# Kernel tuning notes

Hardware: AMD Instinct MI355X
Metric: run time of the kernel (lower is better)

## Reference

```python
import jax, jax.numpy as jnp
import numpy as np

TOPK = 2  # config.expert_topk


def setup_inputs() -> dict:
    key = jax.random.key(0)
    k1, k2, k3, k4 = jax.random.split(key, 4)
    B, T, D, H, E = 2, 2048, 768, 3072, 8
    x = jax.random.normal(k1, (B, T, D), jnp.float32)
    gate_w = jax.random.normal(k2, (E, D), jnp.float32) * 0.02   # nn.Linear(D, E).weight
    w_fc = jax.random.normal(k3, (E, H, D), jnp.float32) * 0.02  # per-expert c_fc.weight [out,in]
    w_proj = jax.random.normal(k4, (E, D, H), jnp.float32) * 0.02  # per-expert c_proj.weight
    return {"x": x, "gate_w": gate_w, "w_fc": w_fc, "w_proj": w_proj}


def reference(x, gate_w, w_fc, w_proj):
    # x: [B,T,D]; gate_w: [E,D]; w_fc: [E,H,D]; w_proj: [E,D,H]
    B, T, D = x.shape
    E = gate_w.shape[0]
    N = B * T
    xf = x.reshape(N, D)

    gate_logits = xf @ gate_w.T                       # [N,E]
    gate_probs = jax.nn.softmax(gate_logits, axis=-1)
    rw, idx = jax.lax.top_k(gate_probs, TOPK)          # [N,k]
    rw = rw / jnp.sum(rw, axis=-1, keepdims=True)

    # combine[n,e] = sum_k rw[n,k] * (idx[n,k]==e); zero for unselected experts,
    # so the dense per-expert MLP below computes the same math as torch dispatch.
    oh = jax.nn.one_hot(idx, E, dtype=xf.dtype)        # [N,k,E]
    combine = jnp.einsum('nk,nke->ne', rw, oh)         # [N,E]

    h = jnp.einsum('nd,ehd->neh', xf, w_fc)            # [N,E,H]
    h = jnp.square(jax.nn.relu(h))                     # relu(x)^2
    y = jnp.einsum('neh,edh->ned', h, w_proj)          # [N,E,D]
    out = jnp.einsum('ned,ne->nd', y, combine).reshape(B, T, D)

    # expert_freq = bincount(expert_indices)/N, detached in the loss
    counts = jnp.sum(oh, axis=(0, 1))                  # [E]
    expert_freq = counts / N
    balance_loss = jnp.sum(gate_probs.mean(axis=0) * jax.lax.stop_gradient(expert_freq)) * E
    return out, balance_loss
```

## Files before the change

kernel.cpp:

```cpp
#include <hip/hip_runtime.h>
#include <hip/hip_bf16.h>

typedef __bf16 bf16_t;
typedef bf16_t bf16x8 __attribute__((ext_vector_type(8)));
typedef bf16_t bf16x4 __attribute__((ext_vector_type(4)));
typedef float f32x4 __attribute__((ext_vector_type(4)));

#define N_TOK 4096
#define DIM   768
#define HID   3072
#define NEXP  8
#define PADROWS 9216
#define MMAX  32
#define MT2   64

#define OFF_COUNTS 0
#define OFF_PSUM   32
#define OFF_OFFPAD 64
#define OFF_CURSOR 128
#define OFF_TOKE   256
#define OFF_TOKW   (OFF_TOKE + 4*8192)
#define OFF_PERMT  (OFF_TOKW + 4*8192)
#define OFF_PERMW  (OFF_PERMT + 4*PADROWS)
#define OFF_XP     (((OFF_PERMW + 4*PADROWS) + 511) & ~511ull)
#define OFF_WFC    (OFF_XP + 2ull*PADROWS*DIM)
#define OFF_WPJ    (OFF_WFC + 2ull*NEXP*HID*DIM)
#define OFF_H      (OFF_WPJ + 2ull*NEXP*DIM*HID)
#define WS_NEEDED  (OFF_H + 2ull*PADROWS*HID)

#define GATE_BLOCKS (N_TOK / 4)
#define CONVH_BLOCKS 4608
#define GEMM1_BLOCKS (8 * 24 * MMAX)

__device__ __forceinline__ void async_copy16(const bf16_t* g, bf16_t* l) {
    __builtin_amdgcn_global_load_lds(
        (const __attribute__((address_space(1))) void*)g,
        (__attribute__((address_space(3))) void*)l, 16, 0, 0);
}

__device__ __forceinline__ void convert_chunk(const float* __restrict__ src,
                                              bf16_t* __restrict__ dst,
                                              int cid, int t) {
    const long long base = (long long)cid * 256 + t;
    const long long stride = (long long)CONVH_BLOCKS * 256;
#pragma unroll
    for (int it = 0; it < 4; it++) {
        const long long i4 = base + (long long)it * stride;
        float4 v = *((const float4*)src + i4);
        bf16x4 o;
        o[0] = (bf16_t)v.x; o[1] = (bf16_t)v.y;
        o[2] = (bf16_t)v.z; o[3] = (bf16_t)v.w;
        *(bf16x4*)(dst + i4 * 4) = o;
    }
}

__global__ __launch_bounds__(256) void prep_kernel(
    const float* __restrict__ w_fc, bf16_t* __restrict__ wfc_b,
    const float* __restrict__ x, const float* __restrict__ gw,
    int* __restrict__ cs_part, float* __restrict__ ps_part,
    int* __restrict__ tok_e, float* __restrict__ tok_w)
{
    __shared__ float ps[8];
    __shared__ int cs[8];

    if (blockIdx.x >= GATE_BLOCKS) {
        convert_chunk(w_fc, wfc_b, blockIdx.x - GATE_BLOCKS, threadIdx.x);
        return;
    }

    if (threadIdx.x < 8) { ps[threadIdx.x] = 0.f; cs[threadIdx.x] = 0; }
    __syncthreads();

    const int bid = blockIdx.x;
    const int wv = threadIdx.x >> 6, lane = threadIdx.x & 63;
    const int n = bid * 4 + wv;

    float acc[8];
#pragma unroll
    for (int e = 0; e < 8; e++) acc[e] = 0.f;
    const float* xr = x + (size_t)n * DIM;
#pragma unroll
    for (int c = 0; c < 12; c++) {
        const float xv = xr[c * 64 + lane];
#pragma unroll
        for (int e = 0; e < 8; e++) acc[e] += xv * gw[e * DIM + c * 64 + lane];
    }
#pragma unroll
    for (int e = 0; e < 8; e++)
        for (int off = 32; off > 0; off >>= 1) acc[e] += __shfl_xor(acc[e], off, 64);

    float mx = acc[0];
#pragma unroll
    for (int e = 1; e < 8; e++) mx = fmaxf(mx, acc[e]);
    float p[8], s = 0.f;
#pragma unroll
    for (int e = 0; e < 8; e++) { p[e] = expf(acc[e] - mx); s += p[e]; }

    int e1 = 0;
#pragma unroll
    for (int e = 1; e < 8; e++) if (p[e] > p[e1]) e1 = e;
    int e2 = (e1 == 0) ? 1 : 0;
#pragma unroll
    for (int e = 0; e < 8; e++) if (e != e1 && p[e] > p[e2]) e2 = e;
    const float denom = p[e1] + p[e2];

    if (lane == 0) {
        tok_e[2 * n] = e1; tok_e[2 * n + 1] = e2;
        tok_w[2 * n] = p[e1] / denom; tok_w[2 * n + 1] = p[e2] / denom;
        const float inv = 1.f / s;
#pragma unroll
        for (int e = 0; e < 8; e++) atomicAdd(&ps[e], p[e] * inv);
        atomicAdd(&cs[e1], 1); atomicAdd(&cs[e2], 1);
    }
    __syncthreads();
    if (threadIdx.x < 8) {
        ps_part[bid * 8 + threadIdx.x] = ps[threadIdx.x];
        cs_part[bid * 8 + threadIdx.x] = cs[threadIdx.x];
    }
}

__global__ __launch_bounds__(256) void finalize_scatter(
    const int* cs_part, const float* ps_part,
    const int* __restrict__ tok_e, const float* __restrict__ tok_w,
    int* __restrict__ counts, int* __restrict__ off_pad,
    int* perm_tok, int* inv_pos, float* __restrict__ out_loss)
{
    __shared__ float rps[256];
    __shared__ int rcs[256];
    __shared__ int s_cur[8];
    const int t = threadIdx.x;
    const int e = t & 7, chunk = t >> 3;
    float psum = 0.f; int csum = 0;
#pragma unroll
    for (int i = 0; i < 32; i++) {
        const int b = chunk * 32 + i;
        psum += ps_part[b * 8 + e];
        csum += cs_part[b * 8 + e];
    }
    rps[t] = psum; rcs[t] = csum;
    __syncthreads();
    for (int s = 128; s >= 8; s >>= 1) {
        if (t < s) { rps[t] += rps[t + s]; rcs[t] += rcs[t + s]; }
        __syncthreads();
    }
    if (t == 0) {
        int off = 0; float loss = 0.f;
        for (int k = 0; k < 8; k++) {
            counts[k] = rcs[k];
            off_pad[k] = off; s_cur[k] = off;
            off += ((rcs[k] + 127) & ~127);
            loss += rps[k] * (float)rcs[k];
        }
        off_pad[8] = off;
        *out_loss = loss * 8.f / ((float)N_TOK * (float)N_TOK);
    }
    __syncthreads();
    for (int r = 0; r < N_TOK / 256; r++) {
        const int n = r * 256 + t;
#pragma unroll
        for (int k = 0; k < 2; k++) {
            const int ee = tok_e[2 * n + k];
            const int pos = atomicAdd(&s_cur[ee], 1);
            perm_tok[pos] = n;
            inv_pos[2 * n + k] = pos;
        }
    }
}

__global__ __launch_bounds__(256) void gather_x_kernel(
    const float* __restrict__ x, const int* __restrict__ off_pad,
    const int* __restrict__ counts, const int* __restrict__ perm_tok,
    bf16_t* __restrict__ xp)
{
    __shared__ int so[9], scnt[8];
    if (threadIdx.x < 9) so[threadIdx.x] = off_pad[threadIdx.x];
    if (threadIdx.x < 8) scnt[threadIdx.x] = counts[threadIdx.x];
    __syncthreads();
    const int gid = blockIdx.x * 256 + threadIdx.x;
    const int p = gid / 192;
    const int c = (gid - p * 192) * 4;
    int e = 0;
#pragma unroll
    for (int k = 1; k < 8; k++) if (p >= so[k]) e = k;
    const bool valid = (p < so[8]) && (p - so[e] < scnt[e]);
    float4 v = make_float4(0.f, 0.f, 0.f, 0.f);
    if (valid) {
        const int tok = perm_tok[p];
        v = *(const float4*)(x + (size_t)tok * DIM + c);
    }
    bf16x4 o; o[0] = (bf16_t)v.x; o[1] = (bf16_t)v.y; o[2] = (bf16_t)v.z; o[3] = (bf16_t)v.w;
    *(bf16x4*)(xp + (size_t)p * DIM + c) = o;
}

__global__ __launch_bounds__(256, 3) void gemm1_kernel(
    const bf16_t* __restrict__ xp, const bf16_t* __restrict__ wfc,
    const int* __restrict__ off_pad, bf16_t* __restrict__ h,
    const float* __restrict__ w_proj, bf16_t* __restrict__ wpj_b)
{
    const int id = blockIdx.x;
    if (id >= GEMM1_BLOCKS) {
        convert_chunk(w_proj, wpj_b, id - GEMM1_BLOCKS, threadIdx.x);
        return;
    }
    const int e = id & 7;
    const int slot = id >> 3;
    const int n_t = slot / MMAX, m_t = slot % MMAX;

    const int seg0 = off_pad[e];
    const int cnt_pad = off_pad[e + 1] - seg0;
    const int m0 = m_t * 128;
    if (m0 >= cnt_pad) return;
    const int n0 = n_t * 128;

    __shared__ bf16_t As[128 * 64];
    __shared__ bf16_t Bs[128 * 64];

    const int t = threadIdx.x;
    const int srow = t >> 3, sc = t & 7;
    const int gsc = sc ^ (srow & 7);
    const bf16_t* abase = xp + (size_t)(seg0 + m0 + srow) * DIM + gsc * 8;
    const bf16_t* bbase = wfc + ((size_t)e * HID + n0 + srow) * DIM + gsc * 8;

    const int wv = t >> 6, lane = t & 63;
    const int lrow = lane & 15, quad = lane >> 4;
    const int wm = (wv & 1) * 64, wn = (wv >> 1) * 64;
    const int sw = lrow & 7;

    f32x4 acc[4][4] = {};

    for (int k0 = 0; k0 < DIM; k0 += 64) {
        __syncthreads();
#pragma unroll
        for (int ii = 0; ii < 4; ii++) {
            async_copy16(abase + (size_t)ii * 32 * DIM + k0, &As[(ii * 256 + t) * 8]);
            async_copy16(bbase + (size_t)ii * 32 * DIM + k0, &Bs[(ii * 256 + t) * 8]);
        }
        __syncthreads();
#pragma unroll
        for (int kh = 0; kh < 2; kh++) {
            const int ch = ((kh * 4 + quad) ^ sw) * 8;
            bf16x8 af[4], bfv[4];
#pragma unroll
            for (int i = 0; i < 4; i++)
                af[i] = *(bf16x8*)&As[(wm + i * 16 + lrow) * 64 + ch];
#pragma unroll
            for (int j = 0; j < 4; j++)
                bfv[j] = *(bf16x8*)&Bs[(wn + j * 16 + lrow) * 64 + ch];
#pragma unroll
            for (int i = 0; i < 4; i++)
#pragma unroll
                for (int j = 0; j < 4; j++)
                    acc[i][j] = __builtin_amdgcn_mfma_f32_16x16x32_bf16(af[i], bfv[j], acc[i][j], 0, 0, 0);
        }
    }

#pragma unroll
    for (int i = 0; i < 4; i++) {
#pragma unroll
        for (int g = 0; g < 4; g++) {
            const int m = m0 + wm + i * 16 + quad * 4 + g;
            bf16_t* hrow = h + (size_t)(seg0 + m) * HID + n0 + wn + lrow;
#pragma unroll
            for (int j = 0; j < 4; j++) {
                float v = fmaxf(acc[i][j][g], 0.f);
                hrow[j * 16] = (bf16_t)(v * v);
            }
        }
    }
}

__global__ __launch_bounds__(256, 3) void gemm2_kernel(
    const bf16_t* __restrict__ h, const bf16_t* __restrict__ wpj,
    const int* __restrict__ off_pad, const int* __restrict__ counts,
    bf16_t* __restrict__ y)
{
    const int id = blockIdx.x;
    const int e = id & 7;
    const int slot = id >> 3;
    const int m_t = slot / 6, n_t = slot % 6;

    const int seg0 = off_pad[e];
    const int cnt = counts[e];
    const int m0 = m_t * 64;
    if (m0 >= cnt) return;
    const int n0 = n_t * 128;

    __shared__ bf16_t As[2][64 * 64];
    __shared__ bf16_t Bs[2][128 * 64];

    const int t = threadIdx.x;
    const int srow = t >> 3, sc = t & 7;
    const int gsc = sc ^ (srow & 7);
    const bf16_t* abase = h + (size_t)(seg0 + m0 + srow) * HID + gsc * 8;
    const bf16_t* bbase = wpj + ((size_t)e * DIM + n0 + srow) * HID + gsc * 8;

    const int wv = t >> 6, lane = t & 63;
    const int lrow = lane & 15, quad = lane >> 4;
    const int wm = (wv & 1) * 32, wn = (wv >> 1) * 64;
    const int sw = lrow & 7;

    f32x4 acc[2][4] = {};

    for (int k0 = 0; k0 < HID; k0 += 128) {
        __syncthreads();
#pragma unroll
        for (int p = 0; p < 2; p++) {
#pragma unroll
            for (int ii = 0; ii < 2; ii++)
                async_copy16(abase + (size_t)ii * 32 * HID + k0 + p * 64,
                             &As[p][(ii * 256 + t) * 8]);
#pragma unroll
            for (int ii = 0; ii < 4; ii++)
                async_copy16(bbase + (size_t)ii * 32 * HID + k0 + p * 64,
                             &Bs[p][(ii * 256 + t) * 8]);
        }
        __syncthreads();
#pragma unroll
        for (int kh = 0; kh < 4; kh++) {
            const int p = kh >> 1, khh = kh & 1;
            const int ch = ((khh * 4 + quad) ^ sw) * 8;
            bf16x8 af[2], bfv[4];
#pragma unroll
            for (int i = 0; i < 2; i++)
                af[i] = *(bf16x8*)&As[p][(wm + i * 16 + lrow) * 64 + ch];
#pragma unroll
            for (int j = 0; j < 4; j++)
                bfv[j] = *(bf16x8*)&Bs[p][(wn + j * 16 + lrow) * 64 + ch];
#pragma unroll
            for (int i = 0; i < 2; i++)
#pragma unroll
                for (int j = 0; j < 4; j++)
                    acc[i][j] = __builtin_amdgcn_mfma_f32_16x16x32_bf16(af[i], bfv[j], acc[i][j], 0, 0, 0);
        }
    }

#pragma unroll
    for (int i = 0; i < 2; i++) {
#pragma unroll
        for (int g = 0; g < 4; g++) {
            const int m = m0 + wm + i * 16 + quad * 4 + g;
            if (m < cnt) {
                bf16_t* yrow = y + (size_t)(seg0 + m) * DIM + n0 + wn + lrow;
#pragma unroll
                for (int j = 0; j < 4; j++)
                    yrow[j * 16] = (bf16_t)acc[i][j][g];
            }
        }
    }
}

__global__ __launch_bounds__(192) void combine_kernel(
    const bf16_t* __restrict__ y, const int* __restrict__ inv_pos,
    const float* __restrict__ tok_w, float* __restrict__ out)
{
    const int n = blockIdx.x;
    const int d = threadIdx.x * 4;
    const int p1 = inv_pos[2 * n], p2 = inv_pos[2 * n + 1];
    const float w1 = tok_w[2 * n], w2 = tok_w[2 * n + 1];
    bf16x4 a = *(const bf16x4*)(y + (size_t)p1 * DIM + d);
    bf16x4 b = *(const bf16x4*)(y + (size_t)p2 * DIM + d);
    float4 o;
    o.x = w1 * (float)a[0] + w2 * (float)b[0];
    o.y = w1 * (float)a[1] + w2 * (float)b[1];
    o.z = w1 * (float)a[2] + w2 * (float)b[2];
    o.w = w1 * (float)a[3] + w2 * (float)b[3];
    *(float4*)(out + (size_t)n * DIM + d) = o;
}

extern "C" void kernel_launch(void* const* d_in, const int* in_sizes, int n_in,
                              void* d_out, int out_size, void* d_ws, size_t ws_size,
                              hipStream_t stream) {
    const float* x      = (const float*)d_in[0];
    const float* gate_w = (const float*)d_in[1];
    const float* w_fc   = (const float*)d_in[2];
    const float* w_proj = (const float*)d_in[3];
    float* out = (float*)d_out;

    if (ws_size < WS_NEEDED) return;

    char* w = (char*)d_ws;
    int*    counts    = (int*)(w + OFF_COUNTS);
    int*    off_pad   = (int*)(w + OFF_OFFPAD);
    int*    tok_e     = (int*)(w + OFF_TOKE);
    float*  tok_w     = (float*)(w + OFF_TOKW);
    int*    perm_tok  = (int*)(w + OFF_PERMT);
    int*    inv_pos   = (int*)(w + OFF_PERMW);
    bf16_t* xp        = (bf16_t*)(w + OFF_XP);
    bf16_t* wfc_b     = (bf16_t*)(w + OFF_WFC);
    bf16_t* wpj_b     = (bf16_t*)(w + OFF_WPJ);
    bf16_t* hbuf      = (bf16_t*)(w + OFF_H);

    int*   cs_part = perm_tok;
    float* ps_part = (float*)inv_pos;
    bf16_t* y = xp;

    hipMemsetAsync(d_out, 0, (size_t)out_size * sizeof(float), stream);

    prep_kernel<<<GATE_BLOCKS + CONVH_BLOCKS, 256, 0, stream>>>(
        w_fc, wfc_b, x, gate_w, cs_part, ps_part, tok_e, tok_w);
    finalize_scatter<<<1, 256, 0, stream>>>(cs_part, ps_part, tok_e, tok_w,
                                            counts, off_pad, perm_tok, inv_pos,
                                            out + (size_t)out_size - 1);
    gather_x_kernel<<<PADROWS * DIM / 4 / 256, 256, 0, stream>>>(x, off_pad, counts, perm_tok, xp);

    gemm1_kernel<<<GEMM1_BLOCKS + CONVH_BLOCKS, 256, 0, stream>>>(
        xp, wfc_b, off_pad, hbuf, w_proj, wpj_b);
    gemm2_kernel<<<8 * MT2 * 6, 256, 0, stream>>>(hbuf, wpj_b, off_pad, counts, y);
    combine_kernel<<<N_TOK, 192, 0, stream>>>(y, inv_pos, tok_w, out);
}
```

Measured before the change: 323.0 us.

## Fuse fp32-to-bf16 weight conversion into GEMM tile loads and drop memset

Removes the separate passes that converted w_fc and w_proj to bf16 in workspace. Each GEMM now reads the fp32 weights directly into registers, converts them, and stores bf16 into LDS, while activations still use async global-to-LDS copies. This skips a full write and re-read of the bf16 weight copies and the extra blocks added to the prep and gemm1 launches. The cost is double the global weight bytes on every tile reload across M tiles, plus register pressure and synchronous loads in the GEMM main loop. The output memset is also dropped, which is only correct if combine_kernel writes every output element.

```diff
diff --git a/kernel.cpp b/kernel.cpp
--- a/kernel.cpp
+++ b/kernel.cpp
@@ -23,13 +23,10 @@
 #define OFF_PERMT  (OFF_TOKW + 4*8192)
 #define OFF_PERMW  (OFF_PERMT + 4*PADROWS)
 #define OFF_XP     (((OFF_PERMW + 4*PADROWS) + 511) & ~511ull)
-#define OFF_WFC    (OFF_XP + 2ull*PADROWS*DIM)
-#define OFF_WPJ    (OFF_WFC + 2ull*NEXP*HID*DIM)
-#define OFF_H      (OFF_WPJ + 2ull*NEXP*DIM*HID)
+#define OFF_H      (OFF_XP + 2ull*PADROWS*DIM)
 #define WS_NEEDED  (OFF_H + 2ull*PADROWS*HID)
 
 #define GATE_BLOCKS (N_TOK / 4)
-#define CONVH_BLOCKS 4608
 #define GEMM1_BLOCKS (8 * 24 * MMAX)
 
 __device__ __forceinline__ void async_copy16(const bf16_t* g, bf16_t* l) {
@@ -38,36 +35,20 @@
         (__attribute__((address_space(3))) void*)l, 16, 0, 0);
 }
 
-__device__ __forceinline__ void convert_chunk(const float* __restrict__ src,
-                                              bf16_t* __restrict__ dst,
-                                              int cid, int t) {
-    const long long base = (long long)cid * 256 + t;
-    const long long stride = (long long)CONVH_BLOCKS * 256;
-#pragma unroll
-    for (int it = 0; it < 4; it++) {
-        const long long i4 = base + (long long)it * stride;
-        float4 v = *((const float4*)src + i4);
-        bf16x4 o;
-        o[0] = (bf16_t)v.x; o[1] = (bf16_t)v.y;
-        o[2] = (bf16_t)v.z; o[3] = (bf16_t)v.w;
-        *(bf16x4*)(dst + i4 * 4) = o;
-    }
-}
-
-__global__ __launch_bounds__(256) void prep_kernel(
-    const float* __restrict__ w_fc, bf16_t* __restrict__ wfc_b,
+__device__ __forceinline__ bf16x8 cvt8(float4 lo, float4 hi) {
+    bf16x8 o;
+    o[0] = (bf16_t)lo.x; o[1] = (bf16_t)lo.y; o[2] = (bf16_t)lo.z; o[3] = (bf16_t)lo.w;
+    o[4] = (bf16_t)hi.x; o[5] = (bf16_t)hi.y; o[6] = (bf16_t)hi.z; o[7] = (bf16_t)hi.w;
+    return o;
+}
+
+__global__ __launch_bounds__(256) void gate_kernel(
     const float* __restrict__ x, const float* __restrict__ gw,
     int* __restrict__ cs_part, float* __restrict__ ps_part,
     int* __restrict__ tok_e, float* __restrict__ tok_w)
 {
     __shared__ float ps[8];
     __shared__ int cs[8];
-
-    if (blockIdx.x >= GATE_BLOCKS) {
-        convert_chunk(w_fc, wfc_b, blockIdx.x - GATE_BLOCKS, threadIdx.x);
-        return;
-    }
-
     if (threadIdx.x < 8) { ps[threadIdx.x] = 0.f; cs[threadIdx.x] = 0; }
     __syncthreads();
 
@@ -193,15 +174,10 @@
 }
 
 __global__ __launch_bounds__(256, 3) void gemm1_kernel(
-    const bf16_t* __restrict__ xp, const bf16_t* __restrict__ wfc,
-    const int* __restrict__ off_pad, bf16_t* __restrict__ h,
-    const float* __restrict__ w_proj, bf16_t* __restrict__ wpj_b)
+    const bf16_t* __restrict__ xp, const float* __restrict__ wfc,
+    const int* __restrict__ off_pad, bf16_t* __restrict__ h)
 {
     const int id = blockIdx.x;
-    if (id >= GEMM1_BLOCKS) {
-        convert_chunk(w_proj, wpj_b, id - GEMM1_BLOCKS, threadIdx.x);
-        return;
-    }
     const int e = id & 7;
     const int slot = id >> 3;
     const int n_t = slot / MMAX, m_t = slot % MMAX;
@@ -219,7 +195,7 @@
     const int srow = t >> 3, sc = t & 7;
     const int gsc = sc ^ (srow & 7);
     const bf16_t* abase = xp + (size_t)(seg0 + m0 + srow) * DIM + gsc * 8;
-    const bf16_t* bbase = wfc + ((size_t)e * HID + n0 + srow) * DIM + gsc * 8;
+    const float*  bbase = wfc + ((size_t)e * HID + n0 + srow) * DIM + gsc * 8;
 
     const int wv = t >> 6, lane = t & 63;
     const int lrow = lane & 15, quad = lane >> 4;
@@ -229,12 +205,20 @@
     f32x4 acc[4][4] = {};
 
     for (int k0 = 0; k0 < DIM; k0 += 64) {
-        __syncthreads();
+        float4 blo[4], bhi[4];
 #pragma unroll
         for (int ii = 0; ii < 4; ii++) {
+            const float* src = bbase + (size_t)ii * 32 * DIM + k0;
+            blo[ii] = *(const float4*)src;
+            bhi[ii] = *(const float4*)(src + 4);
+        }
+        __syncthreads();
+#pragma unroll
+        for (int ii = 0; ii < 4; ii++)
             async_copy16(abase + (size_t)ii * 32 * DIM + k0, &As[(ii * 256 + t) * 8]);
-            async_copy16(bbase + (size_t)ii * 32 * DIM + k0, &Bs[(ii * 256 + t) * 8]);
-        }
+#pragma unroll
+        for (int ii = 0; ii < 4; ii++)
+            *(bf16x8*)&Bs[(ii * 256 + t) * 8] = cvt8(blo[ii], bhi[ii]);
         __syncthreads();
 #pragma unroll
         for (int kh = 0; kh < 2; kh++) {
@@ -270,7 +254,7 @@
 }
 
 __global__ __launch_bounds__(256, 3) void gemm2_kernel(
-    const bf16_t* __restrict__ h, const bf16_t* __restrict__ wpj,
+    const bf16_t* __restrict__ h, const float* __restrict__ wpj,
     const int* __restrict__ off_pad, const int* __restrict__ counts,
     bf16_t* __restrict__ y)
 {
@@ -292,7 +276,7 @@
     const int srow = t >> 3, sc = t & 7;
     const int gsc = sc ^ (srow & 7);
     const bf16_t* abase = h + (size_t)(seg0 + m0 + srow) * HID + gsc * 8;
-    const bf16_t* bbase = wpj + ((size_t)e * DIM + n0 + srow) * HID + gsc * 8;
+    const float*  bbase = wpj + ((size_t)e * DIM + n0 + srow) * HID + gsc * 8;
 
     const int wv = t >> 6, lane = t & 63;
     const int lrow = lane & 15, quad = lane >> 4;
@@ -302,18 +286,27 @@
     f32x4 acc[2][4] = {};
 
     for (int k0 = 0; k0 < HID; k0 += 128) {
-        __syncthreads();
-#pragma unroll
-        for (int p = 0; p < 2; p++) {
+        float4 blo[2][4], bhi[2][4];
+#pragma unroll
+        for (int p = 0; p < 2; p++)
+#pragma unroll
+            for (int ii = 0; ii < 4; ii++) {
+                const float* src = bbase + (size_t)ii * 32 * HID + k0 + p * 64;
+                blo[p][ii] = *(const float4*)src;
+                bhi[p][ii] = *(const float4*)(src + 4);
+            }
+        __syncthreads();
+#pragma unroll
+        for (int p = 0; p < 2; p++)
 #pragma unroll
             for (int ii = 0; ii < 2; ii++)
                 async_copy16(abase + (size_t)ii * 32 * HID + k0 + p * 64,
                              &As[p][(ii * 256 + t) * 8]);
 #pragma unroll
+        for (int p = 0; p < 2; p++)
+#pragma unroll
             for (int ii = 0; ii < 4; ii++)
-                async_copy16(bbase + (size_t)ii * 32 * HID + k0 + p * 64,
-                             &Bs[p][(ii * 256 + t) * 8]);
-        }
+                *(bf16x8*)&Bs[p][(ii * 256 + t) * 8] = cvt8(blo[p][ii], bhi[p][ii]);
         __syncthreads();
 #pragma unroll
         for (int kh = 0; kh < 4; kh++) {
@@ -386,25 +379,19 @@
     int*    perm_tok  = (int*)(w + OFF_PERMT);
     int*    inv_pos   = (int*)(w + OFF_PERMW);
     bf16_t* xp        = (bf16_t*)(w + OFF_XP);
-    bf16_t* wfc_b     = (bf16_t*)(w + OFF_WFC);
-    bf16_t* wpj_b     = (bf16_t*)(w + OFF_WPJ);
     bf16_t* hbuf      = (bf16_t*)(w + OFF_H);
 
     int*   cs_part = perm_tok;
     float* ps_part = (float*)inv_pos;
     bf16_t* y = xp;
 
-    hipMemsetAsync(d_out, 0, (size_t)out_size * sizeof(float), stream);
-
-    prep_kernel<<<GATE_BLOCKS + CONVH_BLOCKS, 256, 0, stream>>>(
-        w_fc, wfc_b, x, gate_w, cs_part, ps_part, tok_e, tok_w);
+    gate_kernel<<<GATE_BLOCKS, 256, 0, stream>>>(x, gate_w, cs_part, ps_part, tok_e, tok_w);
     finalize_scatter<<<1, 256, 0, stream>>>(cs_part, ps_part, tok_e, tok_w,
                                             counts, off_pad, perm_tok, inv_pos,
                                             out + (size_t)out_size - 1);
     gather_x_kernel<<<PADROWS * DIM / 4 / 256, 256, 0, stream>>>(x, off_pad, counts, perm_tok, xp);
 
-    gemm1_kernel<<<GEMM1_BLOCKS + CONVH_BLOCKS, 256, 0, stream>>>(
-        xp, wfc_b, off_pad, hbuf, w_proj, wpj_b);
-    gemm2_kernel<<<8 * MT2 * 6, 256, 0, stream>>>(hbuf, wpj_b, off_pad, counts, y);
+    gemm1_kernel<<<GEMM1_BLOCKS, 256, 0, stream>>>(xp, w_fc, off_pad, hbuf);
+    gemm2_kernel<<<8 * MT2 * 6, 256, 0, stream>>>(hbuf, w_proj, off_pad, counts, y);
     combine_kernel<<<N_TOK, 192, 0, stream>>>(y, inv_pos, tok_w, out);
 }
```

New measurement: 378.5 us. 17.2% more time.
